# Optimization experiments

Hardware: AMD Instinct MI355X
Metric: run time of the kernel (lower is better)

The kernel has to match this reference:

```python
import jax, jax.numpy as jnp
import numpy as np

B, M, D, L = 16384, 16, 128, 26  # words, word length, feature dim, num labels


def setup_inputs() -> dict:
    key = jax.random.key(0)
    k1, k2, k3, k4 = jax.random.split(key, 4)
    X = jax.random.normal(k1, (B, M, D), dtype=jnp.float32)
    Y = jax.random.randint(k2, (B, M), 0, L, dtype=jnp.int64)
    W = jax.random.normal(k3, (L, D), dtype=jnp.float32) * 0.1
    T = jax.random.normal(k4, (L, L), dtype=jnp.float32) * 0.1
    return {"X": X, "Y": Y, "W": W, "T": T}


def reference(X, Y, W, T):
    # Negative conditional log-likelihood of a linear-chain CRF (get_crf_obj).
    # emissions: e[b, s, k] = <W[k], X[b, s]>
    emit = jnp.einsum('bsd,kd->bsk', X, W)  # [B, M, L]
    bsz = X.shape[0]

    # forward recurrence: alpha[i, j] = logsumexp_k(emit[i-1, k] + T[k, j] + alpha[i-1, k])
    def step(alpha, e_prev):
        # alpha, e_prev: [B, L]; T: [L(k), L(j)]
        new = jax.nn.logsumexp(alpha[:, :, None] + e_prev[:, :, None] + T[None, :, :], axis=1)
        return new, None

    alpha0 = jnp.zeros((bsz, emit.shape[-1]), dtype=emit.dtype)
    # scan over positions 0..M-2 (emissions at the previous step)
    alpha_last, _ = jax.lax.scan(step, alpha0, jnp.moveaxis(emit[:, :-1, :], 1, 0))

    # log partition: logsumexp_k(emit[M-1, k] + alpha[M-1, k])
    log_z = jax.nn.logsumexp(emit[:, -1, :] + alpha_last, axis=-1)  # [B]

    # node potential: sum_s emit[s, Y[s]]
    node = jnp.take_along_axis(emit, Y[:, :, None], axis=2)[:, :, 0].sum(axis=1)  # [B]
    # edge potential: sum_s T[Y[s], Y[s+1]]
    edge = T[Y[:, :-1], Y[:, 1:]].sum(axis=1)  # [B]

    log_likelihood = jnp.sum(node + edge - log_z)
    return -log_likelihood
```

## Files before the change

kernel.cpp:

```cpp
#include <hip/hip_runtime.h>
#include <math.h>


#define B_TOT 16384
#define M_LEN 16
#define D_DIM 128
#define L_LAB 26
#define WPB 4
#define NBLOCKS (B_TOT / (WPB * 2))
#define LOG2E 1.4426950408889634f
#define LN2   0.6931471805599453f
#define DELTA 5.7f
#define ESTR 36

typedef short v8s __attribute__((ext_vector_type(8)));
typedef float v4f __attribute__((ext_vector_type(4)));

static __device__ __forceinline__ unsigned bf16u(float f) {
    unsigned u = __float_as_uint(f);
    u += 0x7fff + ((u >> 16) & 1);
    return u >> 16;
}
static __device__ __forceinline__ unsigned pkbf(float lo, float hi) {
    return bf16u(lo) | (bf16u(hi) << 16);
}
static __device__ __forceinline__ float fexp2(float x) {
#if __has_builtin(__builtin_amdgcn_exp2f)
    return __builtin_amdgcn_exp2f(x);
#else
    return exp2f(x);
#endif
}
static __device__ __forceinline__ float flog2(float x) {
#if __has_builtin(__builtin_amdgcn_logf)
    return __builtin_amdgcn_logf(x);
#else
    return log2f(x);
#endif
}

__global__ void prep_kernel(const float* __restrict__ W, const float* __restrict__ T,
                            uint4* __restrict__ wsW, float* __restrict__ wsP) {
    const int l = threadIdx.x;
    const int c16 = l & 15, quad = l >> 4;
    #pragma unroll
    for (int f = 0; f < 8; ++f) {
        const int tile = f >> 2, kk = f & 3;
        const int label = tile * 16 + c16;
        const int base = kk * 32 + quad * 8;
        unsigned d[4];
        #pragma unroll
        for (int p = 0; p < 4; ++p) {
            float a = 0.f, bb = 0.f;
            if (label < L_LAB) {
                a  = W[label * D_DIM + base + 2 * p]     * LOG2E;
                bb = W[label * D_DIM + base + 2 * p + 1] * LOG2E;
            }
            d[p] = pkbf(a, bb);
        }
        wsW[l * 8 + f] = make_uint4(d[0], d[1], d[2], d[3]);
    }
    for (int i = l; i < 1024; i += 64) {
        const int j = i >> 5, k = i & 31;
        wsP[i] = (j < L_LAB && k < L_LAB)
               ? exp2f(T[k * L_LAB + j] * LOG2E - DELTA) : 0.f;
    }
}

__global__ __launch_bounds__(256, 4) void crf_kernel(
    const float* __restrict__ X, const int* __restrict__ Y,
    const float* __restrict__ T, const uint4* __restrict__ wsW,
    const float* __restrict__ wsP, float* __restrict__ out)
{
    const int lane = threadIdx.x & 63;
    const int wave = threadIdx.x >> 6;
    const int g = lane >> 5;
    const int j = lane & 31;
    const int c16 = lane & 15;
    const int quad = lane >> 4;

    __shared__ float Ts[L_LAB * L_LAB];
    __shared__ float Ee[WPB][2][M_LEN * ESTR];
    __shared__ float vrow[WPB][2][32];
    __shared__ float red[WPB];

    for (int i = threadIdx.x; i < L_LAB * L_LAB; i += 256) Ts[i] = T[i];

    uint4 wf[8];
    #pragma unroll
    for (int f = 0; f < 8; ++f) wf[f] = wsW[lane * 8 + f];

    __syncthreads();

    const int wgid = blockIdx.x * WPB + wave;

    #pragma unroll
    for (int g2 = 0; g2 < 2; ++g2) {
        const float* xb = X + (size_t)(wgid * 2 + g2) * (M_LEN * D_DIM);
        v4f acc0 = {0.f, 0.f, 0.f, 0.f};
        v4f acc1 = {0.f, 0.f, 0.f, 0.f};
        #pragma unroll
        for (int kk = 0; kk < 4; ++kk) {
            const float4* xp = (const float4*)(xb + c16 * D_DIM + kk * 32 + quad * 8);
            float4 xa = xp[0];
            float4 xc = xp[1];
            uint4 au = make_uint4(pkbf(xa.x, xa.y), pkbf(xa.z, xa.w),
                                  pkbf(xc.x, xc.y), pkbf(xc.z, xc.w));
            v8s af = *(v8s*)&au;
            v8s b0 = *(v8s*)&wf[kk];
            v8s b1 = *(v8s*)&wf[4 + kk];
            acc0 = __builtin_amdgcn_mfma_f32_16x16x32_bf16(af, b0, acc0, 0, 0, 0);
            acc1 = __builtin_amdgcn_mfma_f32_16x16x32_bf16(af, b1, acc1, 0, 0, 0);
        }
        #pragma unroll
        for (int r = 0; r < 4; ++r) {
            const int s = quad * 4 + r;
            Ee[wave][g2][s * ESTR + c16]      = fexp2(acc0[r]);
            Ee[wave][g2][s * ESTR + 16 + c16] = fexp2(acc1[r]);
        }
    }

    float4 Pc4[7];
    {
        const float4* pp = (const float4*)(wsP + j * 32);
        #pragma unroll
        for (int t = 0; t < 7; ++t) Pc4[t] = pp[t];
    }
    float Ejs[15];
    #pragma unroll
    for (int s = 1; s < M_LEN; ++s) Ejs[s - 1] = Ee[wave][g][s * ESTR + j];

    float ne = 0.f;
    if (j < M_LEN) {
        const int bb = wgid * 2 + g;
        const int ys = Y[bb * M_LEN + j];
        ne = flog2(Ee[wave][g][j * ESTR + ys]) * LN2;
        if (j < M_LEN - 1) {
            const int yn = Y[bb * M_LEN + j + 1];
            ne += Ts[ys * L_LAB + yn];
        }
    }
    ne += __shfl_xor(ne, 8);
    ne += __shfl_xor(ne, 4);
    ne += __shfl_xor(ne, 2);
    ne += __shfl_xor(ne, 1);

    float4 v4[7];
    {
        const float4* e0 = (const float4*)&Ee[wave][g][0];
        #pragma unroll
        for (int t = 0; t < 7; ++t) v4[t] = e0[t];
    }
    #pragma unroll
    for (int s = 1; s < M_LEN; ++s) {
        float4 u4 = make_float4(0.f, 0.f, 0.f, 0.f);
        #pragma unroll
        for (int t = 0; t < 7; ++t) {
            u4.x = fmaf(v4[t].x, Pc4[t].x, u4.x);
            u4.y = fmaf(v4[t].y, Pc4[t].y, u4.y);
            u4.z = fmaf(v4[t].z, Pc4[t].z, u4.z);
            u4.w = fmaf(v4[t].w, Pc4[t].w, u4.w);
        }
        const float u = (u4.x + u4.z) + (u4.y + u4.w);
        vrow[wave][g][j] = u * Ejs[s - 1];
        const float4* vr = (const float4*)&vrow[wave][g][0];
        #pragma unroll
        for (int t = 0; t < 7; ++t) v4[t] = vr[t];
    }

    float4 sv = make_float4(0.f, 0.f, 0.f, 0.f);
    #pragma unroll
    for (int t = 0; t < 7; ++t) {
        sv.x += v4[t].x; sv.y += v4[t].y; sv.z += v4[t].z; sv.w += v4[t].w;
    }
    const float logz = (flog2((sv.x + sv.z) + (sv.y + sv.w)) + 15.f * DELTA) * LN2;

    float local = logz - ne;
    const float other = __shfl(local, 32);
    if (lane == 0) red[wave] = local + other;
    __syncthreads();
    if (threadIdx.x == 0) atomicAdd(out, (red[0] + red[1]) + (red[2] + red[3]));
}

extern "C" void kernel_launch(void* const* d_in, const int* in_sizes, int n_in,
                              void* d_out, int out_size, void* d_ws, size_t ws_size,
                              hipStream_t stream) {
    const float* X = (const float*)d_in[0];
    const int*   Y = (const int*)d_in[1];
    const float* W = (const float*)d_in[2];
    const float* T = (const float*)d_in[3];
    float* out = (float*)d_out;
    uint4* wsW = (uint4*)d_ws;
    float* wsP = (float*)((char*)d_ws + 8192);

    hipMemsetAsync(out, 0, sizeof(float), stream);
    prep_kernel<<<1, 64, 0, stream>>>(W, T, wsW, wsP);
    crf_kernel<<<NBLOCKS, 256, 0, stream>>>(X, Y, T, wsW, wsP, out);
}
```

Measured before the change: 215.5 us.

## Make CRF kernel persistent with double-buffered prefetch of next word pair

Launches a fixed grid of 512 blocks that loop over word pairs instead of one block per 8 words. The X and Y loads for the next pair are issued before the serial forward recurrence of the current pair, with emissions double-buffered in shared memory, so global-memory latency overlaps with compute. It also swaps the manual bf16 rounding for the hardware v_cvt_pk_bf16_f32 instruction and lowers the occupancy hint to 2 blocks per CU. The cost is much higher register pressure from the 16 prefetched float4 values and fewer resident waves to hide latency.

```diff
diff --git a/kernel.cpp b/kernel.cpp
--- a/kernel.cpp
+++ b/kernel.cpp
@@ -7,7 +7,9 @@
 #define D_DIM 128
 #define L_LAB 26
 #define WPB 4
-#define NBLOCKS (B_TOT / (WPB * 2))
+#define NBLK 512
+#define NWAVES (NBLK * WPB)
+#define ITERS (B_TOT / (2 * NWAVES))
 #define LOG2E 1.4426950408889634f
 #define LN2   0.6931471805599453f
 #define DELTA 5.7f
@@ -23,6 +25,11 @@
 }
 static __device__ __forceinline__ unsigned pkbf(float lo, float hi) {
     return bf16u(lo) | (bf16u(hi) << 16);
+}
+static __device__ __forceinline__ unsigned cvtpk(float lo, float hi) {
+    unsigned r;
+    asm("v_cvt_pk_bf16_f32 %0, %1, %2" : "=v"(r) : "v"(lo), "v"(hi));
+    return r;
 }
 static __device__ __forceinline__ float fexp2(float x) {
 #if __has_builtin(__builtin_amdgcn_exp2f)
@@ -67,7 +74,7 @@
     }
 }
 
-__global__ __launch_bounds__(256, 4) void crf_kernel(
+__global__ __launch_bounds__(256, 2) void crf_kernel(
     const float* __restrict__ X, const int* __restrict__ Y,
     const float* __restrict__ T, const uint4* __restrict__ wsW,
     const float* __restrict__ wsP, float* __restrict__ out)
@@ -80,7 +87,7 @@
     const int quad = lane >> 4;
 
     __shared__ float Ts[L_LAB * L_LAB];
-    __shared__ float Ee[WPB][2][M_LEN * ESTR];
+    __shared__ float Ee[WPB][2][2][M_LEN * ESTR];
     __shared__ float vrow[WPB][2][32];
     __shared__ float red[WPB];
 
@@ -89,95 +96,137 @@
     uint4 wf[8];
     #pragma unroll
     for (int f = 0; f < 8; ++f) wf[f] = wsW[lane * 8 + f];
-
-    __syncthreads();
-
-    const int wgid = blockIdx.x * WPB + wave;
-
-    #pragma unroll
-    for (int g2 = 0; g2 < 2; ++g2) {
-        const float* xb = X + (size_t)(wgid * 2 + g2) * (M_LEN * D_DIM);
-        v4f acc0 = {0.f, 0.f, 0.f, 0.f};
-        v4f acc1 = {0.f, 0.f, 0.f, 0.f};
-        #pragma unroll
-        for (int kk = 0; kk < 4; ++kk) {
-            const float4* xp = (const float4*)(xb + c16 * D_DIM + kk * 32 + quad * 8);
-            float4 xa = xp[0];
-            float4 xc = xp[1];
-            uint4 au = make_uint4(pkbf(xa.x, xa.y), pkbf(xa.z, xa.w),
-                                  pkbf(xc.x, xc.y), pkbf(xc.z, xc.w));
-            v8s af = *(v8s*)&au;
-            v8s b0 = *(v8s*)&wf[kk];
-            v8s b1 = *(v8s*)&wf[4 + kk];
-            acc0 = __builtin_amdgcn_mfma_f32_16x16x32_bf16(af, b0, acc0, 0, 0, 0);
-            acc1 = __builtin_amdgcn_mfma_f32_16x16x32_bf16(af, b1, acc1, 0, 0, 0);
-        }
-        #pragma unroll
-        for (int r = 0; r < 4; ++r) {
-            const int s = quad * 4 + r;
-            Ee[wave][g2][s * ESTR + c16]      = fexp2(acc0[r]);
-            Ee[wave][g2][s * ESTR + 16 + c16] = fexp2(acc1[r]);
-        }
-    }
-
     float4 Pc4[7];
     {
         const float4* pp = (const float4*)(wsP + j * 32);
         #pragma unroll
         for (int t = 0; t < 7; ++t) Pc4[t] = pp[t];
     }
-    float Ejs[15];
-    #pragma unroll
-    for (int s = 1; s < M_LEN; ++s) Ejs[s - 1] = Ee[wave][g][s * ESTR + j];
-
-    float ne = 0.f;
-    if (j < M_LEN) {
-        const int bb = wgid * 2 + g;
-        const int ys = Y[bb * M_LEN + j];
-        ne = flog2(Ee[wave][g][j * ESTR + ys]) * LN2;
-        if (j < M_LEN - 1) {
-            const int yn = Y[bb * M_LEN + j + 1];
-            ne += Ts[ys * L_LAB + yn];
-        }
-    }
-    ne += __shfl_xor(ne, 8);
-    ne += __shfl_xor(ne, 4);
-    ne += __shfl_xor(ne, 2);
-    ne += __shfl_xor(ne, 1);
-
-    float4 v4[7];
-    {
-        const float4* e0 = (const float4*)&Ee[wave][g][0];
-        #pragma unroll
-        for (int t = 0; t < 7; ++t) v4[t] = e0[t];
-    }
-    #pragma unroll
-    for (int s = 1; s < M_LEN; ++s) {
-        float4 u4 = make_float4(0.f, 0.f, 0.f, 0.f);
+
+    __syncthreads();
+
+    const int wid = blockIdx.x * WPB + wave;
+
+    float4 px[16];
+    int ysr = 0, ynr = 0;
+    float ne_c = 0.f;
+    float wsum = 0.f;
+
+    auto LOADP = [&](int p) {
+        const float* xr = X + (size_t)p * (2 * M_LEN * D_DIM) + c16 * D_DIM + quad * 8;
+        #pragma unroll
+        for (int g2 = 0; g2 < 2; ++g2) {
+            #pragma unroll
+            for (int kk = 0; kk < 4; ++kk) {
+                const float4* xp = (const float4*)(xr + g2 * (M_LEN * D_DIM) + kk * 32);
+                px[g2 * 8 + kk * 2]     = xp[0];
+                px[g2 * 8 + kk * 2 + 1] = xp[1];
+            }
+        }
+        if (j < M_LEN) {
+            const int bb = p * 2 + g;
+            ysr = Y[bb * M_LEN + j];
+            ynr = (j < M_LEN - 1) ? Y[bb * M_LEN + j + 1] : 0;
+        }
+    };
+
+    auto MFMAP = [&](int buf) {
+        #pragma unroll
+        for (int g2 = 0; g2 < 2; ++g2) {
+            v4f acc0 = {0.f, 0.f, 0.f, 0.f};
+            v4f acc1 = {0.f, 0.f, 0.f, 0.f};
+            #pragma unroll
+            for (int kk = 0; kk < 4; ++kk) {
+                const float4 xa = px[g2 * 8 + kk * 2];
+                const float4 xc = px[g2 * 8 + kk * 2 + 1];
+                uint4 au = make_uint4(cvtpk(xa.x, xa.y), cvtpk(xa.z, xa.w),
+                                      cvtpk(xc.x, xc.y), cvtpk(xc.z, xc.w));
+                v8s af = *(v8s*)&au;
+                v8s b0 = *(v8s*)&wf[kk];
+                v8s b1 = *(v8s*)&wf[4 + kk];
+                acc0 = __builtin_amdgcn_mfma_f32_16x16x32_bf16(af, b0, acc0, 0, 0, 0);
+                acc1 = __builtin_amdgcn_mfma_f32_16x16x32_bf16(af, b1, acc1, 0, 0, 0);
+            }
+            #pragma unroll
+            for (int r = 0; r < 4; ++r) {
+                const int s = quad * 4 + r;
+                Ee[wave][buf][g2][s * ESTR + c16]      = fexp2(acc0[r]);
+                Ee[wave][buf][g2][s * ESTR + 16 + c16] = fexp2(acc1[r]);
+            }
+        }
+    };
+
+    auto NODE = [&](int buf) -> float {
+        float ne = 0.f;
+        if (j < M_LEN) {
+            ne = flog2(Ee[wave][buf][g][j * ESTR + ysr]) * LN2;
+            if (j < M_LEN - 1) ne += Ts[ysr * L_LAB + ynr];
+        }
+        ne += __shfl_xor(ne, 8);
+        ne += __shfl_xor(ne, 4);
+        ne += __shfl_xor(ne, 2);
+        ne += __shfl_xor(ne, 1);
+        return ne;
+    };
+
+    LOADP(wid);
+    MFMAP(0);
+    ne_c = NODE(0);
+
+    for (int it = 0; it < ITERS; ++it) {
+        const int buf = it & 1;
+
+        if (it < ITERS - 1) LOADP((it + 1) * NWAVES + wid);
+        __builtin_amdgcn_sched_barrier(0);
+
+        float Ejs[M_LEN - 1];
+        #pragma unroll
+        for (int s = 1; s < M_LEN; ++s) Ejs[s - 1] = Ee[wave][buf][g][s * ESTR + j];
+
+        float4 v4[7];
+        {
+            const float4* e0 = (const float4*)&Ee[wave][buf][g][0];
+            #pragma unroll
+            for (int t = 0; t < 7; ++t) v4[t] = e0[t];
+        }
+        const float ne = ne_c;
+
+        #pragma unroll
+        for (int s = 1; s < M_LEN; ++s) {
+            float4 u4 = make_float4(0.f, 0.f, 0.f, 0.f);
+            #pragma unroll
+            for (int t = 0; t < 7; ++t) {
+                u4.x = fmaf(v4[t].x, Pc4[t].x, u4.x);
+                u4.y = fmaf(v4[t].y, Pc4[t].y, u4.y);
+                u4.z = fmaf(v4[t].z, Pc4[t].z, u4.z);
+                u4.w = fmaf(v4[t].w, Pc4[t].w, u4.w);
+            }
+            const float u = (u4.x + u4.z) + (u4.y + u4.w);
+            vrow[wave][g][j] = u * Ejs[s - 1];
+            const float4* vr = (const float4*)&vrow[wave][g][0];
+            #pragma unroll
+            for (int t = 0; t < 7; ++t) v4[t] = vr[t];
+        }
+
+        float4 sv = make_float4(0.f, 0.f, 0.f, 0.f);
         #pragma unroll
         for (int t = 0; t < 7; ++t) {
-            u4.x = fmaf(v4[t].x, Pc4[t].x, u4.x);
-            u4.y = fmaf(v4[t].y, Pc4[t].y, u4.y);
-            u4.z = fmaf(v4[t].z, Pc4[t].z, u4.z);
-            u4.w = fmaf(v4[t].w, Pc4[t].w, u4.w);
-        }
-        const float u = (u4.x + u4.z) + (u4.y + u4.w);
-        vrow[wave][g][j] = u * Ejs[s - 1];
-        const float4* vr = (const float4*)&vrow[wave][g][0];
-        #pragma unroll
-        for (int t = 0; t < 7; ++t) v4[t] = vr[t];
-    }
-
-    float4 sv = make_float4(0.f, 0.f, 0.f, 0.f);
-    #pragma unroll
-    for (int t = 0; t < 7; ++t) {
-        sv.x += v4[t].x; sv.y += v4[t].y; sv.z += v4[t].z; sv.w += v4[t].w;
-    }
-    const float logz = (flog2((sv.x + sv.z) + (sv.y + sv.w)) + 15.f * DELTA) * LN2;
-
-    float local = logz - ne;
-    const float other = __shfl(local, 32);
-    if (lane == 0) red[wave] = local + other;
+            sv.x += v4[t].x; sv.y += v4[t].y; sv.z += v4[t].z; sv.w += v4[t].w;
+        }
+        const float logz = (flog2((sv.x + sv.z) + (sv.y + sv.w))
+                            + (float)(M_LEN - 1) * DELTA) * LN2;
+
+        float local = logz - ne;
+        const float other = __shfl(local, 32);
+        if (lane == 0) wsum += local + other;
+
+        if (it < ITERS - 1) {
+            MFMAP(buf ^ 1);
+            ne_c = NODE(buf ^ 1);
+        }
+    }
+
+    if (lane == 0) red[wave] = wsum;
     __syncthreads();
     if (threadIdx.x == 0) atomicAdd(out, (red[0] + red[1]) + (red[2] + red[3]));
 }
@@ -195,5 +244,5 @@
 
     hipMemsetAsync(out, 0, sizeof(float), stream);
     prep_kernel<<<1, 64, 0, stream>>>(W, T, wsW, wsP);
-    crf_kernel<<<NBLOCKS, 256, 0, stream>>>(X, Y, T, wsW, wsP, out);
-}
+    crf_kernel<<<NBLK, 256, 0, stream>>>(X, Y, T, wsW, wsP, out);
+}
```

Result: no change. 211.5 us (-1.9%).
